# Kernel tuning notes

Hardware: AMD Instinct MI355X
Metric: run time of the kernel (lower is better)

Reference implementation:

```python
import jax, jax.numpy as jnp
import numpy as np

LEAKY_ALPHA = 0.2
LN_EPS = 1e-5


def setup_inputs() -> dict:
    key = jax.random.key(0)
    ks = jax.random.split(key, 6)
    B, N, D, R, Hh, hd = 2, 2048, 128, 3, 4, 32  # head_dim = out_dim // num_heads = 128 // 4
    H = jax.random.normal(ks[0], (B, N, D), dtype=jnp.float32)
    A = jax.random.randint(ks[1], (R, B, N, N), 0, 2, dtype=jnp.int32)  # 0/1 adjacency per relation
    w_scale = float(np.sqrt(2.0 / (D + hd)))  # xavier-like
    a_scale = float(np.sqrt(2.0 / (hd + 1)))
    W = jax.random.normal(ks[2], (R, Hh, D, hd), dtype=jnp.float32) * w_scale
    a_src = jax.random.normal(ks[3], (R, Hh, hd), dtype=jnp.float32) * a_scale
    a_dst = jax.random.normal(ks[4], (R, Hh, hd), dtype=jnp.float32) * a_scale
    ln_gamma = jnp.ones((D,), dtype=jnp.float32)
    ln_beta = jnp.zeros((D,), dtype=jnp.float32)
    return {"H": H, "A": A, "W": W, "a_src": a_src, "a_dst": a_dst,
            "ln_gamma": ln_gamma, "ln_beta": ln_beta}


def reference(H, A, W, a_src, a_dst, ln_gamma, ln_beta):
    # H: [B,N,D]; A: [R,B,N,N] int; W: [R,Hh,D,hd]; a_*: [R,Hh,hd]
    R = W.shape[0]
    B, N, D = H.shape
    mask = (A > 0)[:, :, None, :, :]                    # [R,B,1,N,N]
    Wh = jnp.einsum('bnd,rhdf->rbhnf', H, W)             # [R,B,Hh,N,hd]
    e_src = jnp.einsum('rbhnf,rhf->rbhn', Wh, a_src)
    e_dst = jnp.einsum('rbhnf,rhf->rbhn', Wh, a_dst)
    e = e_src[..., :, None] + e_dst[..., None, :]        # [R,B,Hh,N,N]
    e = jax.nn.leaky_relu(e, LEAKY_ALPHA)
    all_false = ~jnp.any(mask, axis=-1, keepdims=True)   # rows with empty neighborhood
    logits = jnp.where(mask, e, -jnp.inf)
    logits = jnp.where(all_false, 0.0, logits)           # avoid NaN on empty rows
    alpha = jax.nn.softmax(logits, axis=-1)
    alpha = jnp.where(all_false, 0.0, alpha)
    # attention-weighted aggregation, mean over relations; -> [B,N,Hh,hd]
    agg = jnp.einsum('rbhij,rbhjf->bihf', alpha, Wh) / R
    out = agg.reshape(B, N, -1)                          # concat heads -> [B,N,out_dim]
    x = H + out                                          # res_proj is Identity (in_dim==out_dim); dropout in eval
    mu = jnp.mean(x, axis=-1, keepdims=True)
    var = jnp.var(x, axis=-1, keepdims=True)
    return (x - mu) / jnp.sqrt(var + LN_EPS) * ln_gamma + ln_beta
```

## Files before the change

### kernel.cpp

```cpp
#include <hip/hip_runtime.h>
#include <hip/hip_bf16.h>

#define RR 3
#define BB 2
#define NN 2048
#define DD 128
#define HH 4
#define HD 32
#define LEAKY 0.2f
#define LN_EPS 1e-5f
#define LOG2E 1.4426950408889634f

using f32x4  = __attribute__((ext_vector_type(4))) float;
using bf16x8 = __attribute__((ext_vector_type(8))) short;

__device__ __forceinline__ void gload_lds16(const void* g, void* l) {
    __builtin_amdgcn_global_load_lds(
        (const __attribute__((address_space(1))) unsigned*)g,
        (__attribute__((address_space(3))) unsigned*)l, 16, 0, 0);
}
__device__ __forceinline__ void gload_lds4(const void* g, void* l) {
    __builtin_amdgcn_global_load_lds(
        (const __attribute__((address_space(1))) unsigned*)g,
        (__attribute__((address_space(3))) unsigned*)l, 4, 0, 0);
}
__device__ __forceinline__ unsigned short bfb(float x) {
    return __builtin_bit_cast(unsigned short, __float2bfloat16(x));
}


__global__ __launch_bounds__(256) void prep_kernel(
    const float* __restrict__ H, const int* __restrict__ A,
    const float* __restrict__ W,
    const float* __restrict__ a_src, const float* __restrict__ a_dst,
    float* __restrict__ es, float* __restrict__ ed,
    __hip_bfloat16* __restrict__ whT, unsigned* __restrict__ bm)
{
    __shared__ unsigned cb_lds[16][65];

    const int bid = blockIdx.x;
    const int t = threadIdx.x;
    const int w = t >> 6;
    const int l = t & 63;

    if (bid < 768) {
        const int sel_e = l >> 3;
        const int sel_q = (l >> 1) & 3;
        const int sel_h = l & 1;
#pragma unroll
        for (int iter = 0; iter < 4; ++iter) {
            const int lr = iter * 4 + w;
            const long crow = (long)bid * 16 + lr;
            const int4* Ap = (const int4*)A + crow * 512 + l;
            int4 v[8];
#pragma unroll
            for (int e = 0; e < 8; ++e) v[e] = Ap[e * 64];
            unsigned word = 0;
#pragma unroll
            for (int e = 0; e < 8; ++e) {
                const unsigned long long B0 = __ballot(v[e].x != 0);
                const unsigned long long B1 = __ballot(v[e].y != 0);
                const unsigned long long B2 = __ballot(v[e].z != 0);
                const unsigned long long B3 = __ballot(v[e].w != 0);
                if (sel_e == e) {
                    const unsigned long long Bq =
                        (sel_q == 3) ? B3 : (sel_q == 2) ? B2 : (sel_q == 1) ? B1 : B0;
                    word = sel_h ? (unsigned)(Bq >> 32) : (unsigned)Bq;
                }
            }
            cb_lds[lr][l] = word;
        }
        __syncthreads();
        {
            const long nrow0g = (long)bid * 16;
            const int rb = (int)(nrow0g >> 11);
            const int nrow0 = (int)(nrow0g & 2047);
            const int p = t >> 2, c = t & 3;
            uint4 val;
            val.x = cb_lds[c * 4 + 0][p];
            val.y = cb_lds[c * 4 + 1][p];
            val.z = cb_lds[c * 4 + 2][p];
            val.w = cb_lds[c * 4 + 3][p];
            *(uint4*)(bm + ((long)rb * 64 + p) * 2048 + nrow0 + c * 4) = val;
        }
        return;
    }

    const int wb = bid - 768;
    const int rbh = wb >> 4;
    const int nch = wb & 15;
    const int h = rbh & 3;
    const int b = (rbh >> 2) & 1;
    const int r = rbh >> 3;
    const int wi = r * HH + h;
    const int lr = l & 15;
    const int lg = l >> 4;

    const float* Wp = W + (long)wi * DD * HD;
    bf16x8 afr[2][4];
#pragma unroll
    for (int mt = 0; mt < 2; ++mt)
#pragma unroll
        for (int kt = 0; kt < 4; ++kt)
#pragma unroll
            for (int e = 0; e < 8; ++e)
                afr[mt][kt][e] = (short)bfb(Wp[(kt * 32 + lg * 8 + e) * HD + mt * 16 + lr]);

    float av[2][4], dv[2][4];
#pragma unroll
    for (int mt = 0; mt < 2; ++mt)
#pragma unroll
        for (int reg = 0; reg < 4; ++reg) {
            const int f = mt * 16 + lg * 4 + reg;
            av[mt][reg] = a_src[wi * HD + f] * LOG2E;
            dv[mt][reg] = a_dst[wi * HD + f] * LOG2E;
        }

    __hip_bfloat16* tile = whT + ((long)rbh * 16 + nch) * 4096;

#pragma unroll
    for (int nt = 0; nt < 2; ++nt) {
        const int ncol = nch * 128 + w * 32 + nt * 16 + lr;
        const float4* hrow4 = (const float4*)(H + ((long)b * NN + ncol) * DD);
        f32x4 acc0 = {0.f, 0.f, 0.f, 0.f};
        f32x4 acc1 = {0.f, 0.f, 0.f, 0.f};
#pragma unroll
        for (int kt = 0; kt < 4; ++kt) {
            float4 h0 = hrow4[kt * 8 + lg * 2];
            float4 h1 = hrow4[kt * 8 + lg * 2 + 1];
            bf16x8 bfr;
            bfr[0] = (short)bfb(h0.x); bfr[1] = (short)bfb(h0.y);
            bfr[2] = (short)bfb(h0.z); bfr[3] = (short)bfb(h0.w);
            bfr[4] = (short)bfb(h1.x); bfr[5] = (short)bfb(h1.y);
            bfr[6] = (short)bfb(h1.z); bfr[7] = (short)bfb(h1.w);
            acc0 = __builtin_amdgcn_mfma_f32_16x16x32_bf16(afr[0][kt], bfr, acc0, 0, 0, 0);
            acc1 = __builtin_amdgcn_mfma_f32_16x16x32_bf16(afr[1][kt], bfr, acc1, 0, 0, 0);
        }
        const int kgw = nt * 2 + (lr >> 3);
        const int ew = lr & 7;
        float s = 0.f, d = 0.f;
#pragma unroll
        for (int reg = 0; reg < 4; ++reg) {
            const int f0 = lg * 4 + reg;
            const int f1 = 16 + lg * 4 + reg;
            tile[((w * 4 + kgw) * 32 + f0) * 8 + ew] = __float2bfloat16(acc0[reg]);
            tile[((w * 4 + kgw) * 32 + f1) * 8 + ew] = __float2bfloat16(acc1[reg]);
            s = fmaf(acc0[reg], av[0][reg], s);
            s = fmaf(acc1[reg], av[1][reg], s);
            d = fmaf(acc0[reg], dv[0][reg], d);
            d = fmaf(acc1[reg], dv[1][reg], d);
        }
        s += __shfl_xor(s, 16); s += __shfl_xor(s, 32);
        d += __shfl_xor(d, 16); d += __shfl_xor(d, 32);
        if (l < 16) {
            es[(long)rbh * NN + ncol] = s;
            ed[(long)rbh * NN + ncol] = d;
        }
    }
}

__global__ __launch_bounds__(256, 3) void gat_attn_kernel(
    const unsigned* __restrict__ bm, const float* __restrict__ es,
    const float* __restrict__ ed, const __hip_bfloat16* __restrict__ whT,
    unsigned* __restrict__ num, float* __restrict__ den)
{
    const int lg = ((int)blockIdx.x % 8) * 96 + (int)blockIdx.x / 8;
    const int jh = lg & 1;
    const int it = (lg >> 1) & 15;
    const int h  = (lg >> 5) & 3;
    const int b  = (lg >> 7) & 1;
    const int r  = lg >> 8;
    const int i0 = it << 7;
    const int tid = threadIdx.x;
    const int w = tid >> 6;
    const int l = tid & 63;
    const int row = l & 15;
    const int kg  = l >> 4;

    __shared__ __align__(16) short    whs[2][4][4][32][8];
    __shared__ __align__(16) unsigned bms[2][4][128];
    __shared__ __align__(16) float    eds[2][4][32];
    __shared__ float red[4];

    const int rbh = (r * BB + b) * HH + h;
    const long rbNN = (long)(r * BB + b) * NN;
    const float* edr = ed + (long)rbh * NN;
    const int jbase = jh * (NN / 2);

#define STAGE(s, nb) do {                                                           \
        const int S_ = jh * 8 + (s);                                                \
        const __hip_bfloat16* tsrc = whT + ((long)rbh * 16 + S_) * 4096;            \
        short* wdst = &whs[nb][0][0][0][0] + w * 1024;                              \
        gload_lds16(tsrc + w * 1024 + l * 8, wdst);                                 \
        gload_lds16(tsrc + w * 1024 + 512 + l * 8, wdst + 512);                     \
        const int woff_ = (S_ >> 1) * 8 + (S_ & 1) + w * 2;                         \
        if (l < 32) gload_lds16(bm + rbNN * 64 + (long)woff_ * 2048 + i0 + l * 4,   \
                                &bms[nb][w][0]);                                    \
        if (l < 32) gload_lds4(edr + jbase + (s) * 128 + w * 32 + l,                \
                               &eds[nb][w][0]);                                     \
    } while (0)

    STAGE(0, 0);

    float4 m0 = ((const float4*)edr)[tid * 2];
    float4 m1 = ((const float4*)edr)[tid * 2 + 1];
    float mm = fmaxf(fmaxf(fmaxf(m0.x, m0.y), fmaxf(m0.z, m0.w)),
                     fmaxf(fmaxf(m1.x, m1.y), fmaxf(m1.z, m1.w)));
#pragma unroll
    for (int d = 1; d < 64; d <<= 1) mm = fmaxf(mm, __shfl_xor(mm, d));
    if (l == 0) red[w] = mm;
    __syncthreads();
    const float medf = fmaxf(fmaxf(red[0], red[1]), fmaxf(red[2], red[3]));

    const float esvA = es[(long)rbh * NN + i0 + w * 16 + row];
    const float esvB = es[(long)rbh * NN + i0 + 64 + w * 16 + row];
    const float xA = esvA + medf, xB = esvB + medf;
    const float MA = fmaxf(xA, LEAKY * xA), MB = fmaxf(xB, LEAKY * xB);
    const float uA = esvA - MA, vA = fmaf(LEAKY, esvA, -MA);
    const float uB = esvB - MB, vB = fmaf(LEAKY, esvB, -MB);

    f32x4 acc0A = {0,0,0,0}, acc1A = {0,0,0,0}, accDA = {0,0,0,0};
    f32x4 acc0B = {0,0,0,0}, acc1B = {0,0,0,0}, accDB = {0,0,0,0};
    bf16x8 ones;
#pragma unroll
    for (int i = 0; i < 8; ++i) ones[i] = (short)0x3F80;

    const int kk = kg * 2;
    const int rAi = w * 16 + row, rBi = 64 + w * 16 + row;

    for (int s = 0; s < 8; ++s) {
        const int cb = s & 1, nb = cb ^ 1;
        if (s < 7) {
            STAGE(s + 1, nb);
            asm volatile("s_waitcnt vmcnt(4)" ::: "memory");
        } else {
            asm volatile("s_waitcnt vmcnt(0)" ::: "memory");
        }
        __builtin_amdgcn_s_barrier();
        __builtin_amdgcn_sched_barrier(0);

        unsigned wA[4], wB[4];
#pragma unroll
        for (int q = 0; q < 4; ++q) {
            wA[q] = bms[cb][q][rAi];
            wB[q] = bms[cb][q][rBi];
        }

#pragma unroll
        for (int jc = 0; jc < 4; ++jc) {
            bf16x8 b0 = *(const bf16x8*)&whs[cb][jc][kg][row][0];
            bf16x8 b1 = *(const bf16x8*)&whs[cb][jc][kg][row + 16][0];
            float4 e0 = *(const float4*)&eds[cb][jc][kg * 8];
            float4 e1 = *(const float4*)&eds[cb][jc][kg * 8 + 4];

            unsigned uAq[4], uBq[4];
#pragma unroll
            for (int q = 0; q < 4; ++q) {
                uAq[q] = wA[q] >> (jc * 8 + kk);
                uBq[q] = wB[q] >> (jc * 8 + kk);
            }

            float ev[8];
            ev[0] = e0.x; ev[1] = e0.y; ev[2] = e0.z; ev[3] = e0.w;
            ev[4] = e1.x; ev[5] = e1.y; ev[6] = e1.z; ev[7] = e1.w;

            bf16x8 pA, pB;
#pragma unroll
            for (int c = 0; c < 8; ++c) {
                float pa = __builtin_amdgcn_exp2f(
                    fmaxf(uA + ev[c], fmaf(LEAKY, ev[c], vA)));
                float pb = __builtin_amdgcn_exp2f(
                    fmaxf(uB + ev[c], fmaf(LEAKY, ev[c], vB)));
                const int ma = ((int)(uAq[c & 3] << (31 - (c >> 2)))) >> 31;
                const int mb = ((int)(uBq[c & 3] << (31 - (c >> 2)))) >> 31;
                pa = __uint_as_float(__float_as_uint(pa) & (unsigned)ma);
                pb = __uint_as_float(__float_as_uint(pb) & (unsigned)mb);
                __hip_bfloat16 ha = __float2bfloat16(pa);
                __hip_bfloat16 hb = __float2bfloat16(pb);
                pA[c] = __builtin_bit_cast(short, ha);
                pB[c] = __builtin_bit_cast(short, hb);
            }

            __builtin_amdgcn_s_setprio(1);
            acc0A = __builtin_amdgcn_mfma_f32_16x16x32_bf16(pA, b0, acc0A, 0, 0, 0);
            acc1A = __builtin_amdgcn_mfma_f32_16x16x32_bf16(pA, b1, acc1A, 0, 0, 0);
            accDA = __builtin_amdgcn_mfma_f32_16x16x32_bf16(pA, ones, accDA, 0, 0, 0);
            acc0B = __builtin_amdgcn_mfma_f32_16x16x32_bf16(pB, b0, acc0B, 0, 0, 0);
            acc1B = __builtin_amdgcn_mfma_f32_16x16x32_bf16(pB, b1, acc1B, 0, 0, 0);
            accDB = __builtin_amdgcn_mfma_f32_16x16x32_bf16(pB, ones, accDB, 0, 0, 0);
            __builtin_amdgcn_s_setprio(0);
        }
        __builtin_amdgcn_s_barrier();
        __builtin_amdgcn_sched_barrier(0);
    }
#undef STAGE

    const int fcol = l & 15;
    const int pr = r * 2 + jh;
#pragma unroll
    for (int reg = 0; reg < 4; ++reg) {
        const int orow = (l >> 4) * 4 + reg;
        const long roA = (long)pr * (BB * NN) + (long)b * NN + i0 + w * 16 + orow;
        const long roB = roA + 64;
        const unsigned wa = (unsigned)bfb(acc0A[reg]) | ((unsigned)bfb(acc1A[reg]) << 16);
        const unsigned wb_ = (unsigned)bfb(acc0B[reg]) | ((unsigned)bfb(acc1B[reg]) << 16);
        num[roA * 64 + h * 16 + fcol] = wa;
        num[roB * 64 + h * 16 + fcol] = wb_;
        if (fcol == 0) {
            den[roA * HH + h] = accDA[reg];
            den[roB * HH + h] = accDB[reg];
        }
    }
}

__global__ __launch_bounds__(256) void finalize_kernel(
    const float* __restrict__ H, const unsigned* __restrict__ num,
    const float* __restrict__ den,
    const float* __restrict__ gamma, const float* __restrict__ beta,
    float* __restrict__ out)
{
    const int w = threadIdx.x >> 6;
    const int l = threadIdx.x & 63;
    const long row = (long)blockIdx.x * 4 + w;
    const int hh = l >> 4, cc = l & 15;
    const int c_lo = hh * 32 + cc, c_hi = c_lo + 16;
    const float hx = H[row * DD + c_lo];
    const float hy = H[row * DD + c_hi];

    float ax = 0.f, ay = 0.f;
#pragma unroll
    for (int r = 0; r < RR; ++r) {
        float dsum = 0.f, nx = 0.f, ny = 0.f;
#pragma unroll
        for (int j = 0; j < 2; ++j) {
            const long ro = (long)(r * 2 + j) * (BB * NN) + row;
            dsum += den[ro * HH + hh];
            const unsigned wv = num[ro * 64 + l];
            nx += __uint_as_float(wv << 16);
            ny += __uint_as_float(wv & 0xffff0000u);
        }
        const float inv = (dsum > 0.f) ? 1.0f / dsum : 0.0f;
        ax = fmaf(nx, inv, ax);
        ay = fmaf(ny, inv, ay);
    }
    const float x0 = hx + ax * (1.0f / RR);
    const float x1 = hy + ay * (1.0f / RR);
    float s = x0 + x1, q = x0 * x0 + x1 * x1;
#pragma unroll
    for (int m = 1; m < 64; m <<= 1) {
        s += __shfl_xor(s, m);
        q += __shfl_xor(q, m);
    }
    const float mu  = s * (1.0f / DD);
    const float var = q * (1.0f / DD) - mu * mu;
    const float inv = rsqrtf(var + LN_EPS);
    out[row * DD + c_lo] = (x0 - mu) * inv * gamma[c_lo] + beta[c_lo];
    out[row * DD + c_hi] = (x1 - mu) * inv * gamma[c_hi] + beta[c_hi];
}

extern "C" void kernel_launch(void* const* d_in, const int* in_sizes, int n_in,
                              void* d_out, int out_size, void* d_ws, size_t ws_size,
                              hipStream_t stream)
{
    const float* H      = (const float*)d_in[0];
    const int*   A      = (const int*)d_in[1];
    const float* W      = (const float*)d_in[2];
    const float* a_src  = (const float*)d_in[3];
    const float* a_dst  = (const float*)d_in[4];
    const float* gamma  = (const float*)d_in[5];
    const float* beta   = (const float*)d_in[6];
    float* out = (float*)d_out;

    char* ws = (char*)d_ws;
    unsigned* num = (unsigned*)ws;               ws += (size_t)RR * 2 * BB * NN * 64 * 4;
    float* den = (float*)ws;                     ws += (size_t)RR * 2 * BB * NN * HH * 4;
    float* es  = (float*)ws;                     ws += (size_t)RR * BB * HH * NN * 4;
    float* ed  = (float*)ws;                     ws += (size_t)RR * BB * HH * NN * 4;
    __hip_bfloat16* whT = (__hip_bfloat16*)ws;   ws += (size_t)RR * BB * HH * HD * NN * 2;
    unsigned* bmask = (unsigned*)ws;             ws += (size_t)RR * BB * NN * (NN / 32) * 4;

    prep_kernel<<<768 + 384, 256, 0, stream>>>(
        H, A, W, a_src, a_dst, es, ed, whT, bmask);
    gat_attn_kernel<<<RR * BB * HH * 16 * 2, 256, 0, stream>>>(bmask, es, ed, whT, num, den);
    finalize_kernel<<<BB * NN / 4, 256, 0, stream>>>(H, num, den, gamma, beta, out);
}
```

Before: 64.71 us.

## Restructure attention kernel to one head per wave with direct global loads

Each block now covers 16 query rows across all four heads, one wave per head, instead of 128 rows of a single head. The LDS double-buffered staging and barriers are removed, so each wave reads whT, the bitmask and ed straight from global memory (cached), and occupancy is raised to 6 blocks per SIMD pool. This drops synchronisation and LDS traffic and gives more blocks, but each wave loses the reuse of B-operand tiles across 128 rows, which increases global and cache traffic per row.

```diff
diff --git a/kernel.cpp b/kernel.cpp
--- a/kernel.cpp
+++ b/kernel.cpp
@@ -14,16 +14,6 @@
 using f32x4  = __attribute__((ext_vector_type(4))) float;
 using bf16x8 = __attribute__((ext_vector_type(8))) short;
 
-__device__ __forceinline__ void gload_lds16(const void* g, void* l) {
-    __builtin_amdgcn_global_load_lds(
-        (const __attribute__((address_space(1))) unsigned*)g,
-        (__attribute__((address_space(3))) unsigned*)l, 16, 0, 0);
-}
-__device__ __forceinline__ void gload_lds4(const void* g, void* l) {
-    __builtin_amdgcn_global_load_lds(
-        (const __attribute__((address_space(1))) unsigned*)g,
-        (__attribute__((address_space(3))) unsigned*)l, 4, 0, 0);
-}
 __device__ __forceinline__ unsigned short bfb(float x) {
     return __builtin_bit_cast(unsigned short, __float2bfloat16(x));
 }
@@ -159,157 +149,104 @@
     }
 }
 
-__global__ __launch_bounds__(256, 3) void gat_attn_kernel(
+__global__ __launch_bounds__(256, 6) void gat_attn_kernel(
     const unsigned* __restrict__ bm, const float* __restrict__ es,
     const float* __restrict__ ed, const __hip_bfloat16* __restrict__ whT,
     unsigned* __restrict__ num, float* __restrict__ den)
 {
-    const int lg = ((int)blockIdx.x % 8) * 96 + (int)blockIdx.x / 8;
+    const int lg = ((int)blockIdx.x % 8) * 192 + (int)blockIdx.x / 8;
     const int jh = lg & 1;
-    const int it = (lg >> 1) & 15;
-    const int h  = (lg >> 5) & 3;
-    const int b  = (lg >> 7) & 1;
-    const int r  = lg >> 8;
-    const int i0 = it << 7;
+    const int it = (lg >> 1) & 127;
+    const int b  = (lg >> 8) & 1;
+    const int r  = lg >> 9;
+    const int i0 = it << 4;
     const int tid = threadIdx.x;
-    const int w = tid >> 6;
+    const int h = tid >> 6;
     const int l = tid & 63;
     const int row = l & 15;
     const int kg  = l >> 4;
 
-    __shared__ __align__(16) short    whs[2][4][4][32][8];
-    __shared__ __align__(16) unsigned bms[2][4][128];
-    __shared__ __align__(16) float    eds[2][4][32];
-    __shared__ float red[4];
-
-    const int rbh = (r * BB + b) * HH + h;
-    const long rbNN = (long)(r * BB + b) * NN;
+    const int rb  = r * BB + b;
+    const int rbh = rb * HH + h;
     const float* edr = ed + (long)rbh * NN;
-    const int jbase = jh * (NN / 2);
-
-#define STAGE(s, nb) do {                                                           \
-        const int S_ = jh * 8 + (s);                                                \
-        const __hip_bfloat16* tsrc = whT + ((long)rbh * 16 + S_) * 4096;            \
-        short* wdst = &whs[nb][0][0][0][0] + w * 1024;                              \
-        gload_lds16(tsrc + w * 1024 + l * 8, wdst);                                 \
-        gload_lds16(tsrc + w * 1024 + 512 + l * 8, wdst + 512);                     \
-        const int woff_ = (S_ >> 1) * 8 + (S_ & 1) + w * 2;                         \
-        if (l < 32) gload_lds16(bm + rbNN * 64 + (long)woff_ * 2048 + i0 + l * 4,   \
-                                &bms[nb][w][0]);                                    \
-        if (l < 32) gload_lds4(edr + jbase + (s) * 128 + w * 32 + l,                \
-                               &eds[nb][w][0]);                                     \
-    } while (0)
-
-    STAGE(0, 0);
-
-    float4 m0 = ((const float4*)edr)[tid * 2];
-    float4 m1 = ((const float4*)edr)[tid * 2 + 1];
-    float mm = fmaxf(fmaxf(fmaxf(m0.x, m0.y), fmaxf(m0.z, m0.w)),
-                     fmaxf(fmaxf(m1.x, m1.y), fmaxf(m1.z, m1.w)));
+
+    float mm = -1e30f;
+#pragma unroll
+    for (int k = 0; k < 8; ++k) {
+        float4 v = ((const float4*)edr)[k * 64 + l];
+        mm = fmaxf(mm, fmaxf(fmaxf(v.x, v.y), fmaxf(v.z, v.w)));
+    }
 #pragma unroll
     for (int d = 1; d < 64; d <<= 1) mm = fmaxf(mm, __shfl_xor(mm, d));
-    if (l == 0) red[w] = mm;
-    __syncthreads();
-    const float medf = fmaxf(fmaxf(red[0], red[1]), fmaxf(red[2], red[3]));
-
-    const float esvA = es[(long)rbh * NN + i0 + w * 16 + row];
-    const float esvB = es[(long)rbh * NN + i0 + 64 + w * 16 + row];
-    const float xA = esvA + medf, xB = esvB + medf;
-    const float MA = fmaxf(xA, LEAKY * xA), MB = fmaxf(xB, LEAKY * xB);
-    const float uA = esvA - MA, vA = fmaf(LEAKY, esvA, -MA);
-    const float uB = esvB - MB, vB = fmaf(LEAKY, esvB, -MB);
-
-    f32x4 acc0A = {0,0,0,0}, acc1A = {0,0,0,0}, accDA = {0,0,0,0};
-    f32x4 acc0B = {0,0,0,0}, acc1B = {0,0,0,0}, accDB = {0,0,0,0};
+
+    const float esv = es[(long)rbh * NN + i0 + row];
+    const float x = esv + mm;
+    const float M = fmaxf(x, LEAKY * x);
+    const float uA = esv - M;
+    const float vA = fmaf(LEAKY, esv, -M);
+
+    f32x4 acc0 = {0,0,0,0}, acc1 = {0,0,0,0}, accD = {0,0,0,0};
     bf16x8 ones;
 #pragma unroll
     for (int i = 0; i < 8; ++i) ones[i] = (short)0x3F80;
 
     const int kk = kg * 2;
-    const int rAi = w * 16 + row, rBi = 64 + w * 16 + row;
-
-    for (int s = 0; s < 8; ++s) {
-        const int cb = s & 1, nb = cb ^ 1;
-        if (s < 7) {
-            STAGE(s + 1, nb);
-            asm volatile("s_waitcnt vmcnt(4)" ::: "memory");
-        } else {
-            asm volatile("s_waitcnt vmcnt(0)" ::: "memory");
-        }
-        __builtin_amdgcn_s_barrier();
-        __builtin_amdgcn_sched_barrier(0);
-
-        unsigned wA[4], wB[4];
-#pragma unroll
-        for (int q = 0; q < 4; ++q) {
-            wA[q] = bms[cb][q][rAi];
-            wB[q] = bms[cb][q][rBi];
-        }
+    const unsigned* bmb = bm + (long)rb * 64 * 2048 + i0 + row;
+
+#pragma unroll 1
+    for (int seg = 0; seg < 8; ++seg) {
+        const int S = jh * 8 + seg;
+        const __hip_bfloat16* tile = whT + ((long)rbh * 16 + S) * 4096;
+        const int wbase = (S >> 1) * 8 + (S & 1);
+        unsigned wA[4];
+#pragma unroll
+        for (int q = 0; q < 4; ++q)
+            wA[q] = bmb[(long)(wbase + q * 2) * 2048];
+        const float* edseg = edr + S * 128;
 
 #pragma unroll
         for (int jc = 0; jc < 4; ++jc) {
-            bf16x8 b0 = *(const bf16x8*)&whs[cb][jc][kg][row][0];
-            bf16x8 b1 = *(const bf16x8*)&whs[cb][jc][kg][row + 16][0];
-            float4 e0 = *(const float4*)&eds[cb][jc][kg * 8];
-            float4 e1 = *(const float4*)&eds[cb][jc][kg * 8 + 4];
-
-            unsigned uAq[4], uBq[4];
-#pragma unroll
-            for (int q = 0; q < 4; ++q) {
-                uAq[q] = wA[q] >> (jc * 8 + kk);
-                uBq[q] = wB[q] >> (jc * 8 + kk);
-            }
+            bf16x8 b0 = *(const bf16x8*)(tile + jc * 1024 + kg * 256 + row * 8);
+            bf16x8 b1 = *(const bf16x8*)(tile + jc * 1024 + kg * 256 + 128 + row * 8);
+            float4 e0 = *(const float4*)(edseg + jc * 32 + kg * 8);
+            float4 e1 = *(const float4*)(edseg + jc * 32 + kg * 8 + 4);
+
+            unsigned uq[4];
+#pragma unroll
+            for (int q = 0; q < 4; ++q) uq[q] = wA[q] >> (jc * 8 + kk);
 
             float ev[8];
             ev[0] = e0.x; ev[1] = e0.y; ev[2] = e0.z; ev[3] = e0.w;
             ev[4] = e1.x; ev[5] = e1.y; ev[6] = e1.z; ev[7] = e1.w;
 
-            bf16x8 pA, pB;
+            bf16x8 p;
 #pragma unroll
             for (int c = 0; c < 8; ++c) {
                 float pa = __builtin_amdgcn_exp2f(
                     fmaxf(uA + ev[c], fmaf(LEAKY, ev[c], vA)));
-                float pb = __builtin_amdgcn_exp2f(
-                    fmaxf(uB + ev[c], fmaf(LEAKY, ev[c], vB)));
-                const int ma = ((int)(uAq[c & 3] << (31 - (c >> 2)))) >> 31;
-                const int mb = ((int)(uBq[c & 3] << (31 - (c >> 2)))) >> 31;
+                const int ma = ((int)(uq[c & 3] << (31 - (c >> 2)))) >> 31;
                 pa = __uint_as_float(__float_as_uint(pa) & (unsigned)ma);
-                pb = __uint_as_float(__float_as_uint(pb) & (unsigned)mb);
                 __hip_bfloat16 ha = __float2bfloat16(pa);
-                __hip_bfloat16 hb = __float2bfloat16(pb);
-                pA[c] = __builtin_bit_cast(short, ha);
-                pB[c] = __builtin_bit_cast(short, hb);
+                p[c] = __builtin_bit_cast(short, ha);
             }
 
             __builtin_amdgcn_s_setprio(1);
-            acc0A = __builtin_amdgcn_mfma_f32_16x16x32_bf16(pA, b0, acc0A, 0, 0, 0);
-            acc1A = __builtin_amdgcn_mfma_f32_16x16x32_bf16(pA, b1, acc1A, 0, 0, 0);
-            accDA = __builtin_amdgcn_mfma_f32_16x16x32_bf16(pA, ones, accDA, 0, 0, 0);
-            acc0B = __builtin_amdgcn_mfma_f32_16x16x32_bf16(pB, b0, acc0B, 0, 0, 0);
-            acc1B = __builtin_amdgcn_mfma_f32_16x16x32_bf16(pB, b1, acc1B, 0, 0, 0);
-            accDB = __builtin_amdgcn_mfma_f32_16x16x32_bf16(pB, ones, accDB, 0, 0, 0);
+            acc0 = __builtin_amdgcn_mfma_f32_16x16x32_bf16(p, b0, acc0, 0, 0, 0);
+            acc1 = __builtin_amdgcn_mfma_f32_16x16x32_bf16(p, b1, acc1, 0, 0, 0);
+            accD = __builtin_amdgcn_mfma_f32_16x16x32_bf16(p, ones, accD, 0, 0, 0);
             __builtin_amdgcn_s_setprio(0);
         }
-        __builtin_amdgcn_s_barrier();
-        __builtin_amdgcn_sched_barrier(0);
-    }
-#undef STAGE
+    }
 
     const int fcol = l & 15;
     const int pr = r * 2 + jh;
 #pragma unroll
     for (int reg = 0; reg < 4; ++reg) {
         const int orow = (l >> 4) * 4 + reg;
-        const long roA = (long)pr * (BB * NN) + (long)b * NN + i0 + w * 16 + orow;
-        const long roB = roA + 64;
-        const unsigned wa = (unsigned)bfb(acc0A[reg]) | ((unsigned)bfb(acc1A[reg]) << 16);
-        const unsigned wb_ = (unsigned)bfb(acc0B[reg]) | ((unsigned)bfb(acc1B[reg]) << 16);
-        num[roA * 64 + h * 16 + fcol] = wa;
-        num[roB * 64 + h * 16 + fcol] = wb_;
-        if (fcol == 0) {
-            den[roA * HH + h] = accDA[reg];
-            den[roB * HH + h] = accDB[reg];
-        }
+        const long ro = (long)pr * (BB * NN) + (long)b * NN + i0 + orow;
+        num[ro * 64 + h * 16 + fcol] =
+            (unsigned)bfb(acc0[reg]) | ((unsigned)bfb(acc1[reg]) << 16);
+        if (fcol == 0) den[ro * HH + h] = accD[reg];
     }
 }
 
@@ -381,6 +318,6 @@
 
     prep_kernel<<<768 + 384, 256, 0, stream>>>(
         H, A, W, a_src, a_dst, es, ed, whT, bmask);
-    gat_attn_kernel<<<RR * BB * HH * 16 * 2, 256, 0, stream>>>(bmask, es, ed, whT, num, den);
+    gat_attn_kernel<<<RR * BB * 128 * 2, 256, 0, stream>>>(bmask, es, ed, whT, num, den);
     finalize_kernel<<<BB * NN / 4, 256, 0, stream>>>(H, num, den, gamma, beta, out);
 }
```

After: 63.40 us (median of 2 runs). 2.0% less time.
